# Kernel optimization log

Measured on AMD Instinct MI355X. Metric: run time of the kernel, lower is better.

Reference implementation:

```python
import jax, jax.numpy as jnp
import numpy as np

N = 8192            # number of ROIs
FEAT = 255          # num_classes(151) + embed_dim(100) + pos_dim(4)
HID = 64
PRE_NMS = 6000      # eval-mode pre_nms_topn
POST_NMS = 300      # eval-mode post_nms_topn
NMS_THRESH = 0.7


def setup_inputs() -> dict:
    key = jax.random.key(0)
    ks = jax.random.split(key, 12)
    # rois: [N,5] = (im_ind, x1, y1, x2, y2), valid boxes in a 1024x1024 image
    x1 = jax.random.uniform(ks[0], (N,)) * 900.0
    y1 = jax.random.uniform(ks[1], (N,)) * 900.0
    w = jax.random.uniform(ks[2], (N,)) * 120.0 + 4.0
    h = jax.random.uniform(ks[3], (N,)) * 120.0 + 4.0
    rois = jnp.stack([jnp.zeros((N,)), x1, y1, x1 + w, y1 + h], axis=1).astype(jnp.float32)
    roi_feat = jax.random.normal(ks[4], (N, FEAT), dtype=jnp.float32)
    s = 0.05
    return {
        "rois": rois,
        "roi_feat": roi_feat,
        "W_sub1": jax.random.normal(ks[5], (FEAT, HID), jnp.float32) * s,
        "b_sub1": jnp.zeros((HID,), jnp.float32),
        "W_sub2": jax.random.normal(ks[6], (HID, HID), jnp.float32) * s,
        "b_sub2": jnp.zeros((HID,), jnp.float32),
        "W_obj1": jax.random.normal(ks[7], (FEAT, HID), jnp.float32) * s,
        "b_obj1": jnp.zeros((HID,), jnp.float32),
        "W_obj2": jax.random.normal(ks[8], (HID, HID), jnp.float32) * s,
        "b_obj2": jnp.zeros((HID,), jnp.float32),
    }


def _iou_matrix(boxes):
    # boxes: [K,4] (x1,y1,x2,y2) -> [K,K] IoU
    x1, y1, x2, y2 = boxes[:, 0], boxes[:, 1], boxes[:, 2], boxes[:, 3]
    area = (x2 - x1) * (y2 - y1)
    ix1 = jnp.maximum(x1[:, None], x1[None, :])
    iy1 = jnp.maximum(y1[:, None], y1[None, :])
    ix2 = jnp.minimum(x2[:, None], x2[None, :])
    iy2 = jnp.minimum(y2[:, None], y2[None, :])
    inter = jnp.maximum(ix2 - ix1, 0.0) * jnp.maximum(iy2 - iy1, 0.0)
    return inter / (area[:, None] + area[None, :] - inter + 1e-8)


def reference(rois, roi_feat, W_sub1, b_sub1, W_sub2, b_sub2,
              W_obj1, b_obj1, W_obj2, b_obj2):
    # Original detaches roi_feat before the bilinear head.
    f = jax.lax.stop_gradient(roi_feat)
    x_sub = jnp.maximum(f @ W_sub1 + b_sub1, 0.0) @ W_sub2 + b_sub2  # [N,64]
    x_obj = jnp.maximum(f @ W_obj1 + b_obj1, 0.0) @ W_obj2 + b_obj2  # [N,64]
    scores = jax.nn.sigmoid(x_sub @ x_obj.T)                          # [N,N]

    n = scores.shape[0]
    # exclude self-pairs (sub == obj)
    diag = jnp.arange(n)
    flat = scores.at[diag, diag].set(-1.0).reshape(-1)

    # pre-NMS top-k over all N*N pairs (sorted descending)
    top_s, top_i = jax.lax.top_k(flat, PRE_NMS)
    sub = top_i // n
    obj = top_i % n

    boxes = jax.lax.stop_gradient(rois[:, 1:5])
    bs, bo = boxes[sub], boxes[obj]
    # union box of each (sub,obj) pair for relation NMS
    union = jnp.concatenate([jnp.minimum(bs[:, :2], bo[:, :2]),
                             jnp.maximum(bs[:, 2:], bo[:, 2:])], axis=1)  # [PRE,4]
    iou = _iou_matrix(union)                                              # [PRE,PRE]
    # non-greedy (matrix) NMS: suppress i if any higher-ranked j overlaps > thresh
    higher = jnp.triu(jnp.ones((PRE_NMS, PRE_NMS), bool), k=1)  # [j,i] true when j < i
    suppressed = jnp.any((iou > NMS_THRESH) & higher, axis=0)
    kept_scores = jnp.where(suppressed, -1.0, top_s)

    post_s, post_k = jax.lax.top_k(kept_scores, POST_NMS)
    rel_inds = jnp.stack([sub[post_k], obj[post_k]], axis=1)  # [POST,2]
    return rel_inds, post_s
```

## Files before the change

### kernel.cpp

```cpp
#include <hip/hip_runtime.h>
#include <math.h>

#define NB    8192
#define FEAT  255
#define HID   64
#define TOPK  6000
#define POSTK 300
#define BINS  8192
#define BSHIFT 19
#define CAP   131072
#define CAPLIM 49152
#define SLACK 1
#define TSEL  500
#define SAMPF 16
#define JSLICES 128
#define LCAP  2048
#define NMS_ICH 64

typedef __attribute__((ext_vector_type(8))) short bf16x8;
typedef __attribute__((ext_vector_type(4))) float f32x4;
typedef __attribute__((ext_vector_type(4))) double f64x4;

__device__ __forceinline__ unsigned binOf(float x) {
    unsigned u = __float_as_uint(x);
    u = (u & 0x80000000u) ? ~u : (u | 0x80000000u);
    return u >> BSHIFT;
}

__device__ __forceinline__ unsigned short f2bf(float f) {
    unsigned u = __float_as_uint(f);
    return (unsigned short)((u + 0x7fffu + ((u >> 16) & 1u)) >> 16);
}

__global__ __launch_bounds__(256) void mlp_kernel(
    const float* __restrict__ feat,
    const float* __restrict__ W1s, const float* __restrict__ b1s,
    const float* __restrict__ W2s, const float* __restrict__ b2s,
    const float* __restrict__ W1o, const float* __restrict__ b1o,
    const float* __restrict__ W2o, const float* __restrict__ b2o,
    double* __restrict__ Xs64, double* __restrict__ Xo64,
    unsigned short* __restrict__ Xsb, unsigned short* __restrict__ Xob)
{
    __shared__ float  fl[16 * 258];
    __shared__ double hl[2][16][65];

    int tid  = threadIdx.x;
    int lane = tid & 63;
    int w    = tid >> 6;
    int a16  = lane & 15;
    int kq   = lane >> 4;
    int net  = w & 1;
    int p    = w >> 1;
    int rbase = blockIdx.x * 16;

    const float* fsrc = feat + (size_t)rbase * FEAT;
    for (int idx = tid; idx < 16 * FEAT; idx += 256) {
        int r = idx / FEAT;
        int k = idx - r * FEAT;
        fl[r * 258 + k] = fsrc[idx];
    }
    if (tid < 16) fl[tid * 258 + 255] = 0.0f;
    __syncthreads();

    const float* W1 = net ? W1o : W1s;
    const float* B1 = net ? b1o : b1s;
    const float* W2 = net ? W2o : W2s;
    const float* B2 = net ? b2o : b2s;
    double*       X  = net ? Xo64 : Xs64;
    unsigned short* Xb = net ? Xob : Xsb;

    int c0 = (2 * p) * 16 + a16;
    int c1 = (2 * p + 1) * 16 + a16;

    f64x4 acc0 = {0, 0, 0, 0}, acc1 = {0, 0, 0, 0};
#pragma unroll 4
    for (int ks = 0; ks < 63; ++ks) {
        int k = ks * 4 + kq;
        double av = (double)fl[a16 * 258 + k];
        double b0 = (double)W1[k * HID + c0];
        double b1 = (double)W1[k * HID + c1];
        acc0 = __builtin_amdgcn_mfma_f64_16x16x4f64(av, b0, acc0, 0, 0, 0);
        acc1 = __builtin_amdgcn_mfma_f64_16x16x4f64(av, b1, acc1, 0, 0, 0);
    }
    {
        int k = 252 + kq;
        double av = (double)fl[a16 * 258 + k];
        double b0 = 0.0, b1 = 0.0;
        if (k < FEAT) {
            b0 = (double)W1[k * HID + c0];
            b1 = (double)W1[k * HID + c1];
        }
        acc0 = __builtin_amdgcn_mfma_f64_16x16x4f64(av, b0, acc0, 0, 0, 0);
        acc1 = __builtin_amdgcn_mfma_f64_16x16x4f64(av, b1, acc1, 0, 0, 0);
    }

    {
        double bb0 = (double)B1[c0], bb1 = (double)B1[c1];
#pragma unroll
        for (int i = 0; i < 4; ++i) {
            int r = kq * 4 + i;
            double v0 = acc0[i] + bb0;
            double v1 = acc1[i] + bb1;
            hl[net][r][c0] = v0 > 0.0 ? v0 : 0.0;
            hl[net][r][c1] = v1 > 0.0 ? v1 : 0.0;
        }
    }
    __syncthreads();

    f64x4 x0 = {0, 0, 0, 0}, x1 = {0, 0, 0, 0};
#pragma unroll 4
    for (int ks = 0; ks < 16; ++ks) {
        int k = ks * 4 + kq;
        double av = hl[net][a16][k];
        double b0 = (double)W2[k * HID + c0];
        double b1 = (double)W2[k * HID + c1];
        x0 = __builtin_amdgcn_mfma_f64_16x16x4f64(av, b0, x0, 0, 0, 0);
        x1 = __builtin_amdgcn_mfma_f64_16x16x4f64(av, b1, x1, 0, 0, 0);
    }

    {
        double bb0 = (double)B2[c0], bb1 = (double)B2[c1];
#pragma unroll
        for (int i = 0; i < 4; ++i) {
            int r = kq * 4 + i;
            double v0 = x0[i] + bb0;
            double v1 = x1[i] + bb1;
            size_t o0 = (size_t)(rbase + r) * HID + c0;
            size_t o1 = (size_t)(rbase + r) * HID + c1;
            X[o0] = v0; X[o1] = v1;
            Xb[o0] = f2bf((float)v0);
            Xb[o1] = f2bf((float)v1);
        }
    }
}

__global__ __launch_bounds__(256) void mfma_hist(
    const unsigned short* __restrict__ Xsb, const unsigned short* __restrict__ Xob,
    unsigned* __restrict__ ghist, unsigned* __restrict__ ctrl)
{
    __shared__ unsigned hist[BINS];
    __shared__ unsigned csum[256];
    __shared__ bool win_s;
    int tid = threadIdx.x;
    for (int i = tid; i < BINS; i += 256) hist[i] = 0u;
    __syncthreads();

    int lane = tid & 63;
    int wave = tid >> 6;
    int quad = lane >> 4;
    int l16  = lane & 15;
    int r0 = blockIdx.y * 128 + (wave >> 1) * 64;
    int c0 = blockIdx.x * 128 + (wave & 1) * 64;

    f32x4 acc[4][4];
    bf16x8 afr[2][4], bfr[2][4];
#pragma unroll
    for (int kc = 0; kc < 2; ++kc)
#pragma unroll
        for (int t = 0; t < 4; ++t) {
            afr[kc][t] = *(const bf16x8*)(Xsb + (size_t)(r0 + t * 16 + l16) * HID + kc * 32 + quad * 8);
            bfr[kc][t] = *(const bf16x8*)(Xob + (size_t)(c0 + t * 16 + l16) * HID + kc * 32 + quad * 8);
        }
#pragma unroll
    for (int ti = 0; ti < 4; ++ti)
#pragma unroll
        for (int tj = 0; tj < 4; ++tj) acc[ti][tj] = (f32x4){0, 0, 0, 0};
#pragma unroll
    for (int kc = 0; kc < 2; ++kc)
#pragma unroll
        for (int ti = 0; ti < 4; ++ti)
#pragma unroll
            for (int tj = 0; tj < 4; ++tj)
                acc[ti][tj] = __builtin_amdgcn_mfma_f32_16x16x32_bf16(
                    afr[kc][ti], bfr[kc][tj], acc[ti][tj], 0, 0, 0);

#pragma unroll
    for (int ti = 0; ti < 4; ++ti)
#pragma unroll
        for (int tj = 0; tj < 4; ++tj)
#pragma unroll
            for (int i = 0; i < 4; ++i) {
                int r = r0 + ti * 16 + quad * 4 + i;
                int c = c0 + tj * 16 + l16;
                float v = acc[ti][tj][i];
                if (v > 0.0f && r != c)
                    atomicAdd(&hist[binOf(v)], 1u);
            }

    __syncthreads();
    for (int i = tid; i < BINS; i += 256) {
        unsigned h = hist[i];
        if (h) atomicAdd(&ghist[i], h);
    }

    __syncthreads();
    if (tid == 0) {
        __threadfence();
        unsigned done = atomicAdd(&ctrl[3], 1u);
        win_s = (done == gridDim.x * gridDim.y - 1u);
    }
    __syncthreads();
    if (!win_s) return;

    for (int i = tid; i < BINS; i += 256)
        hist[i] = __hip_atomic_load(&ghist[i], __ATOMIC_RELAXED, __HIP_MEMORY_SCOPE_AGENT);
    __syncthreads();

    int base = tid * (BINS / 256);
    unsigned s = 0;
    for (int i = 0; i < BINS / 256; ++i) s += hist[base + i];
    csum[tid] = s;
    __syncthreads();
    if (tid == 0) {
        unsigned run = 0;
        for (int c = 255; c >= 0; --c) { run += csum[c]; csum[c] = run; }
    }
    __syncthreads();

    unsigned above = (tid == 255) ? 0u : csum[tid + 1];
    unsigned prev = above;
    for (int b = base + BINS / 256 - 1; b >= base; --b) {
        unsigned cur = prev + hist[b];
        if (cur >= TSEL && prev < TSEL) {
            unsigned bstar = (unsigned)b;
            unsigned bt = bstar >= SLACK ? bstar - SLACK : 0;
            unsigned cnt = cur;
            for (unsigned bb = bstar; bb-- > bt;) cnt += hist[bb];
            while ((unsigned)SAMPF * cnt > CAPLIM && bt < bstar) { cnt -= hist[bt]; bt++; }
            ctrl[1] = bt;
            unsigned key = bt << BSHIFT;
            unsigned fbits;
            if (key == 0u) fbits = 0xff800000u;
            else fbits = (key & 0x80000000u) ? (key ^ 0x80000000u) : ~key;
            ctrl[2] = fbits;
            break;
        }
        prev = cur;
    }
}

__global__ __launch_bounds__(256) void mfma_filter(
    const unsigned short* __restrict__ Xsb, const unsigned short* __restrict__ Xob,
    unsigned* __restrict__ ctrl, unsigned* __restrict__ cidx)
{
    __shared__ unsigned lcnt;
    __shared__ unsigned gbase;
    __shared__ unsigned lbuf[LCAP];
    float vt = __uint_as_float(ctrl[2]);
    int tid = threadIdx.x;
    if (tid == 0) lcnt = 0;

    int lane = tid & 63;
    int wave = tid >> 6;
    int quad = lane >> 4;
    int l16  = lane & 15;
    int r0 = blockIdx.y * 128 + (wave >> 1) * 64;
    int cb = blockIdx.x * 256 + (wave & 1) * 64;

    bf16x8 afr[2][4];
#pragma unroll
    for (int kc = 0; kc < 2; ++kc)
#pragma unroll
        for (int t = 0; t < 4; ++t)
            afr[kc][t] = *(const bf16x8*)(Xsb + (size_t)(r0 + t * 16 + l16) * HID + kc * 32 + quad * 8);

    bf16x8 b0[2], b1[2];
    {
        int col0 = cb + l16;
        int col1 = cb + 16 + l16;
#pragma unroll
        for (int kc = 0; kc < 2; ++kc) {
            b0[kc] = *(const bf16x8*)(Xob + (size_t)col0 * HID + kc * 32 + quad * 8);
            b1[kc] = *(const bf16x8*)(Xob + (size_t)col1 * HID + kc * 32 + quad * 8);
        }
    }

    __syncthreads();

#pragma unroll
    for (int q = 0; q < 8; ++q) {
        int ct = q >> 2, tj = q & 3;
        int c0 = cb + ct * 128;
        int cj = c0 + tj * 16 + l16;
        bool nodiag = (r0 != c0);

        bf16x8 b2[2];
        if (q < 6) {
            int q2 = q + 2;
            int col2 = cb + (q2 >> 2) * 128 + (q2 & 3) * 16 + l16;
#pragma unroll
            for (int kc = 0; kc < 2; ++kc)
                b2[kc] = *(const bf16x8*)(Xob + (size_t)col2 * HID + kc * 32 + quad * 8);
        }

        f32x4 acc[4];
#pragma unroll
        for (int ti = 0; ti < 4; ++ti) acc[ti] = (f32x4){0, 0, 0, 0};
#pragma unroll
        for (int kc = 0; kc < 2; ++kc)
#pragma unroll
            for (int ti = 0; ti < 4; ++ti)
                acc[ti] = __builtin_amdgcn_mfma_f32_16x16x32_bf16(
                    afr[kc][ti], b0[kc], acc[ti], 0, 0, 0);

        unsigned hm = 0u;
#pragma unroll
        for (int ti = 0; ti < 4; ++ti)
#pragma unroll
            for (int i = 0; i < 4; ++i) {
                bool hit = acc[ti][i] >= vt;
                if (!nodiag) {
                    int r = r0 + ti * 16 + quad * 4 + i;
                    hit = hit && (r != cj);
                }
                hm |= hit ? (1u << (ti * 4 + i)) : 0u;
            }

        if (__any(hm != 0u)) {
#pragma unroll
            for (int ti = 0; ti < 4; ++ti)
#pragma unroll
                for (int i = 0; i < 4; ++i) {
                    if (hm & (1u << (ti * 4 + i))) {
                        int r = r0 + ti * 16 + quad * 4 + i;
                        unsigned rc = (unsigned)r * (unsigned)NB + (unsigned)cj;
                        unsigned p = atomicAdd(&lcnt, 1u);
                        if (p < LCAP) {
                            lbuf[p] = rc;
                        } else {
                            unsigned g = atomicAdd(&ctrl[0], 1u);
                            if (g < CAP) cidx[g] = rc;
                        }
                    }
                }
        }

        if (q < 6) {
            b0[0] = b1[0]; b0[1] = b1[1];
            b1[0] = b2[0]; b1[1] = b2[1];
        } else if (q == 6) {
            b0[0] = b1[0]; b0[1] = b1[1];
        }
    }

    __syncthreads();
    unsigned n = lcnt; if (n > LCAP) n = LCAP;
    if (tid == 0 && n) gbase = atomicAdd(&ctrl[0], n);
    __syncthreads();
    for (unsigned i = tid; i < n; i += 256u) {
        unsigned p = gbase + i;
        if (p < CAP) cidx[p] = lbuf[i];
    }
}

__global__ __launch_bounds__(256) void refine_kernel(
    const unsigned* __restrict__ ctrl, const unsigned* __restrict__ cidx,
    const double* __restrict__ Xs64, const double* __restrict__ Xo64,
    double* __restrict__ cval)
{
    unsigned M = ctrl[0];
    if (M > CAP) M = CAP;
    unsigned nw = gridDim.x * 4u;
    int lane = threadIdx.x & 63;
    for (unsigned w = blockIdx.x * 4u + (threadIdx.x >> 6); w < M; w += nw) {
        unsigned id = cidx[w];
        unsigned r = id >> 13, c = id & (NB - 1);
        double p = Xs64[(size_t)r * HID + lane] * Xo64[(size_t)c * HID + lane];
#pragma unroll
        for (int s = 32; s > 0; s >>= 1) p += __shfl_xor(p, s);
        if (lane == 0) cval[w] = (r == c) ? -1.0 : p;
    }
}

__global__ __launch_bounds__(256) void rank_count(
    const unsigned* __restrict__ ctrl,
    const double* __restrict__ cval, const unsigned* __restrict__ cidx,
    unsigned* __restrict__ rank)
{
    unsigned M = ctrl[0];
    if (M > CAP) M = CAP;

    unsigned slice = blockIdx.y;
    unsigned jbeg = (unsigned)(((unsigned long long)slice * M) / JSLICES);
    unsigned jend = (unsigned)(((unsigned long long)(slice + 1) * M) / JSLICES);

    __shared__ double  lv[256];
    __shared__ unsigned li[256];

    for (unsigned itile = blockIdx.x; itile * 1024u < M; itile += gridDim.x) {
        unsigned i0 = itile * 1024u + threadIdx.x;
        double v[4];
        unsigned id[4];
        unsigned cnt[4] = {0, 0, 0, 0};
#pragma unroll
        for (int k = 0; k < 4; ++k) {
            unsigned idx = i0 + (unsigned)k * 256u;
            bool a = idx < M;
            v[k]  = a ? cval[idx] : 0.0;
            id[k] = a ? cidx[idx] : 0u;
        }

        for (unsigned base = jbeg; base < jend; base += 256u) {
            unsigned j = base + threadIdx.x;
            if (j < jend) { lv[threadIdx.x] = cval[j]; li[threadIdx.x] = cidx[j]; }
            __syncthreads();
            unsigned lim = jend - base; if (lim > 256u) lim = 256u;
            for (unsigned e = 0; e < lim; ++e) {
                double ev = lv[e];
                unsigned ei = li[e];
#pragma unroll
                for (int k = 0; k < 4; ++k)
                    cnt[k] += (ev > v[k]) || (ev == v[k] && ei < id[k]);
            }
            __syncthreads();
        }
#pragma unroll
        for (int k = 0; k < 4; ++k) {
            unsigned idx = i0 + (unsigned)k * 256u;
            if (idx < M && cnt[k]) atomicAdd(&rank[idx], cnt[k]);
        }
    }
}

__global__ __launch_bounds__(256) void rank_scatter_prep(
    const unsigned* __restrict__ ctrl,
    const double* __restrict__ cval, const unsigned* __restrict__ cidx,
    const unsigned* __restrict__ rank, const float* __restrict__ rois,
    double* __restrict__ sval, unsigned* __restrict__ sidx,
    double* __restrict__ ub)
{
    unsigned M = ctrl[0];
    if (M > CAP) M = CAP;
    unsigned stride = gridDim.x * 256u;
    for (unsigned t = blockIdx.x * 256u + threadIdx.x; t < M; t += stride) {
        unsigned rk = rank[t];
        if (rk < TOPK) {
            unsigned id = cidx[t];
            sval[rk] = cval[t];
            sidx[rk] = id;
            unsigned s = id >> 13, o = id & (NB - 1);
            const float* bs = rois + (size_t)s * 5;
            const float* bo = rois + (size_t)o * 5;
            double x1 = fmin((double)bs[1], (double)bo[1]);
            double y1 = fmin((double)bs[2], (double)bo[2]);
            double x2 = fmax((double)bs[3], (double)bo[3]);
            double y2 = fmax((double)bs[4], (double)bo[4]);
            double area = (x2 - x1) * (y2 - y1);
            double* u = ub + (size_t)rk * 5;
            u[0] = x1; u[1] = y1; u[2] = x2; u[3] = y2; u[4] = 0.7 * area;
        }
    }
}

__global__ __launch_bounds__(256) void nms_kernel(
    const double* __restrict__ ub, unsigned* sup)
{
    int jb = blockIdx.x;
    int ic = blockIdx.y;
    int ibase = ic * NMS_ICH;
    if (ibase >= TOPK) return;
    if (ibase >= jb * 256 + 255) return;

    __shared__ double L[NMS_ICH][5];
    int tid = threadIdx.x;
    int icount = TOPK - ibase; if (icount > NMS_ICH) icount = NMS_ICH;
    for (int q = tid; q < icount * 5; q += 256)
        L[q / 5][q % 5] = ub[(size_t)ibase * 5 + q];
    __syncthreads();

    int j = jb * 256 + tid;
    if (j >= TOPK) return;
    int lim = j - ibase; if (lim > icount) lim = icount;
    if (lim <= 0) return;

    const double* u = ub + (size_t)j * 5;
    double x1 = u[0], y1 = u[1], x2 = u[2], y2 = u[3], pa = u[4];
    bool flag = false;
    for (int e = 0; e < lim; ++e) {
        double ix1 = fmax(L[e][0], x1);
        double iy1 = fmax(L[e][1], y1);
        double ix2 = fmin(L[e][2], x2);
        double iy2 = fmin(L[e][3], y2);
        double iw = ix2 - ix1; iw = iw > 0.0 ? iw : 0.0;
        double ih = iy2 - iy1; ih = ih > 0.0 ? ih : 0.0;
        flag |= (1.7 * (iw * ih) > pa + L[e][4] + 7e-9);
    }
    if (flag) sup[j] = 1u;
}

__global__ __launch_bounds__(1024) void finalize_kernel(
    const unsigned* __restrict__ sup, const double* __restrict__ sval,
    const unsigned* __restrict__ sidx, float* __restrict__ out)
{
    __shared__ unsigned wsum[16];
    __shared__ unsigned red[16];
    __shared__ unsigned bases[2];
    __shared__ unsigned totalu_s;
    int tid  = threadIdx.x;
    int lane = tid & 63;
    int w    = tid >> 6;

    unsigned s = 0;
    for (int i = tid; i < TOPK; i += 1024) s += (sup[i] == 0u);
#pragma unroll
    for (int st = 32; st > 0; st >>= 1) s += __shfl_down(s, st);
    if (lane == 0) red[w] = s;
    __syncthreads();
    if (tid == 0) {
        unsigned tot = 0;
        for (int i = 0; i < 16; ++i) tot += red[i];
        totalu_s = tot; bases[0] = 0; bases[1] = 0;
    }
    __syncthreads();
    unsigned totalu = totalu_s;

    for (int c = 0; c < (TOPK + 1023) / 1024; ++c) {
        int idx = c * 1024 + tid;
        int valid = TOPK - c * 1024; if (valid > 1024) valid = 1024;
        unsigned f = (idx < TOPK && sup[idx] == 0u) ? 1u : 0u;
        unsigned long long m = __ballot(f != 0u);
        if (lane == 0) wsum[w] = (unsigned)__popcll(m);
        __syncthreads();
        unsigned wbase = 0, ctot = 0;
        for (int i = 0; i < 16; ++i) {
            unsigned v = wsum[i];
            if (i < w) wbase += v;
            ctot += v;
        }
        unsigned e = wbase + (unsigned)__popcll(m & ((1ull << lane) - 1ull));
        if (idx < TOPK) {
            unsigned pos = f ? (bases[0] + e)
                             : (totalu + bases[1] + (unsigned)tid - e);
            if (pos < POSTK) {
                unsigned id = sidx[idx];
                unsigned sb = id >> 13, ob = id & (NB - 1);
                out[2 * pos]     = (float)sb;
                out[2 * pos + 1] = (float)ob;
                double sg = f ? 1.0 / (1.0 + exp(-sval[idx])) : -1.0;
                out[2 * POSTK + pos] = (float)sg;
            }
        }
        __syncthreads();
        if (tid == 0) {
            bases[0] += ctot;
            bases[1] += (unsigned)valid - ctot;
        }
        __syncthreads();
    }
}

extern "C" void kernel_launch(void* const* d_in, const int* in_sizes, int n_in,
                              void* d_out, int out_size, void* d_ws, size_t ws_size,
                              hipStream_t stream)
{
    const float* rois = (const float*)d_in[0];
    const float* feat = (const float*)d_in[1];
    const float* W1s  = (const float*)d_in[2];
    const float* b1s  = (const float*)d_in[3];
    const float* W2s  = (const float*)d_in[4];
    const float* b2s  = (const float*)d_in[5];
    const float* W1o  = (const float*)d_in[6];
    const float* b1o  = (const float*)d_in[7];
    const float* W2o  = (const float*)d_in[8];
    const float* b2o  = (const float*)d_in[9];

    char* ws = (char*)d_ws;
    size_t off = 0;
    auto alloc = [&](size_t bytes) -> void* {
        off = (off + 255) & ~(size_t)255;
        void* p = ws + off;
        off += bytes;
        return p;
    };

    unsigned* ghist = (unsigned*)alloc((size_t)BINS * 4);
    unsigned* ctrl  = (unsigned*)alloc(256);
    unsigned* sup   = (unsigned*)alloc((size_t)6144 * 4);
    unsigned* rank  = (unsigned*)alloc((size_t)CAP * 4);
    size_t zero_bytes = off;

    double* Xs64 = (double*)alloc((size_t)NB * HID * 8);
    double* Xo64 = (double*)alloc((size_t)NB * HID * 8);
    unsigned short* Xsb = (unsigned short*)alloc((size_t)NB * HID * 2);
    unsigned short* Xob = (unsigned short*)alloc((size_t)NB * HID * 2);
    double* cval = (double*)alloc((size_t)CAP * 8);
    unsigned* cidx = (unsigned*)alloc((size_t)CAP * 4);
    double* svalv = (double*)alloc((size_t)TOPK * 8);
    unsigned* sidxv = (unsigned*)alloc((size_t)TOPK * 4);
    double* ub   = (double*)alloc((size_t)TOPK * 5 * 8);

    hipMemsetAsync(d_ws, 0, zero_bytes, stream);

    mlp_kernel<<<NB / 16, 256, 0, stream>>>(feat, W1s, b1s, W2s, b2s,
                                            W1o, b1o, W2o, b2o,
                                            Xs64, Xo64, Xsb, Xob);
    mfma_hist<<<dim3(4, 64), 256, 0, stream>>>(Xsb, Xob, ghist, ctrl);
    mfma_filter<<<dim3(32, 64), 256, 0, stream>>>(Xsb, Xob, ctrl, cidx);
    refine_kernel<<<2048, 256, 0, stream>>>(ctrl, cidx, Xs64, Xo64, cval);
    rank_count<<<dim3(16, JSLICES), 256, 0, stream>>>(ctrl, cval, cidx, rank);
    rank_scatter_prep<<<512, 256, 0, stream>>>(ctrl, cval, cidx, rank, rois,
                                               svalv, sidxv, ub);
    nms_kernel<<<dim3((TOPK + 255) / 256, (TOPK + NMS_ICH - 1) / NMS_ICH), 256, 0, stream>>>(ub, sup);
    finalize_kernel<<<1, 1024, 0, stream>>>(sup, svalv, sidxv, (float*)d_out);
}
```

Before: 225.3 us.

## Fuse refine, scatter and finalize stages into neighbouring kernels via last-block pattern

Candidate double-precision rescoring moves into the filter kernel, so each block refines the candidates it just appended; rank zeroing is also done there and drops out of the memset. The rank scatter and union-box prep now run in the last-finishing block of rank_count, found through an atomic counter. Finalize likewise runs in the last-finishing block of the NMS kernel. This removes three kernel launches and their inter-kernel gaps. In exchange, the scatter and finalize work is serialized onto one 256-thread block, and correctness depends on threadfence and atomic visibility.

```diff
diff --git a/kernel.cpp b/kernel.cpp
--- a/kernel.cpp
+++ b/kernel.cpp
@@ -241,7 +241,9 @@
 
 __global__ __launch_bounds__(256) void mfma_filter(
     const unsigned short* __restrict__ Xsb, const unsigned short* __restrict__ Xob,
-    unsigned* __restrict__ ctrl, unsigned* __restrict__ cidx)
+    unsigned* __restrict__ ctrl, unsigned* __restrict__ cidx,
+    const double* __restrict__ Xs64, const double* __restrict__ Xo64,
+    double* __restrict__ cval, unsigned* __restrict__ rank)
 {
     __shared__ unsigned lcnt;
     __shared__ unsigned gbase;
@@ -329,7 +331,15 @@
                             lbuf[p] = rc;
                         } else {
                             unsigned g = atomicAdd(&ctrl[0], 1u);
-                            if (g < CAP) cidx[g] = rc;
+                            if (g < CAP) {
+                                cidx[g] = rc;
+                                const double* xr = Xs64 + (size_t)r * HID;
+                                const double* xc = Xo64 + (size_t)cj * HID;
+                                double a64 = 0.0;
+                                for (int k = 0; k < HID; ++k) a64 += xr[k] * xc[k];
+                                cval[g] = a64;
+                                rank[g] = 0u;
+                            }
                         }
                     }
                 }
@@ -351,34 +361,29 @@
         unsigned p = gbase + i;
         if (p < CAP) cidx[p] = lbuf[i];
     }
-}
-
-__global__ __launch_bounds__(256) void refine_kernel(
-    const unsigned* __restrict__ ctrl, const unsigned* __restrict__ cidx,
-    const double* __restrict__ Xs64, const double* __restrict__ Xo64,
-    double* __restrict__ cval)
+
+    for (unsigned i = (unsigned)wave; i < n; i += 4u) {
+        unsigned g = gbase + i;
+        if (g < CAP) {
+            unsigned rc = lbuf[i];
+            unsigned r = rc >> 13, c = rc & (NB - 1u);
+            double pr = Xs64[(size_t)r * HID + lane] * Xo64[(size_t)c * HID + lane];
+#pragma unroll
+            for (int s = 32; s > 0; s >>= 1) pr += __shfl_xor(pr, s);
+            if (lane == 0) { cval[g] = pr; rank[g] = 0u; }
+        }
+    }
+}
+
+__global__ __launch_bounds__(256) void rank_count(
+    unsigned* __restrict__ ctrl,
+    const double* __restrict__ cval, const unsigned* __restrict__ cidx,
+    unsigned* __restrict__ rank, const float* __restrict__ rois,
+    double* __restrict__ sval, unsigned* __restrict__ sidx,
+    double* __restrict__ ub)
 {
     unsigned M = ctrl[0];
     if (M > CAP) M = CAP;
-    unsigned nw = gridDim.x * 4u;
-    int lane = threadIdx.x & 63;
-    for (unsigned w = blockIdx.x * 4u + (threadIdx.x >> 6); w < M; w += nw) {
-        unsigned id = cidx[w];
-        unsigned r = id >> 13, c = id & (NB - 1);
-        double p = Xs64[(size_t)r * HID + lane] * Xo64[(size_t)c * HID + lane];
-#pragma unroll
-        for (int s = 32; s > 0; s >>= 1) p += __shfl_xor(p, s);
-        if (lane == 0) cval[w] = (r == c) ? -1.0 : p;
-    }
-}
-
-__global__ __launch_bounds__(256) void rank_count(
-    const unsigned* __restrict__ ctrl,
-    const double* __restrict__ cval, const unsigned* __restrict__ cidx,
-    unsigned* __restrict__ rank)
-{
-    unsigned M = ctrl[0];
-    if (M > CAP) M = CAP;
 
     unsigned slice = blockIdx.y;
     unsigned jbeg = (unsigned)(((unsigned long long)slice * M) / JSLICES);
@@ -386,6 +391,7 @@
 
     __shared__ double  lv[256];
     __shared__ unsigned li[256];
+    __shared__ bool win_s;
 
     for (unsigned itile = blockIdx.x; itile * 1024u < M; itile += gridDim.x) {
         unsigned i0 = itile * 1024u + threadIdx.x;
@@ -420,20 +426,18 @@
             if (idx < M && cnt[k]) atomicAdd(&rank[idx], cnt[k]);
         }
     }
-}
-
-__global__ __launch_bounds__(256) void rank_scatter_prep(
-    const unsigned* __restrict__ ctrl,
-    const double* __restrict__ cval, const unsigned* __restrict__ cidx,
-    const unsigned* __restrict__ rank, const float* __restrict__ rois,
-    double* __restrict__ sval, unsigned* __restrict__ sidx,
-    double* __restrict__ ub)
-{
-    unsigned M = ctrl[0];
-    if (M > CAP) M = CAP;
-    unsigned stride = gridDim.x * 256u;
-    for (unsigned t = blockIdx.x * 256u + threadIdx.x; t < M; t += stride) {
-        unsigned rk = rank[t];
+
+    __syncthreads();
+    if (threadIdx.x == 0) {
+        __threadfence();
+        unsigned done = atomicAdd(&ctrl[4], 1u);
+        win_s = (done == gridDim.x * gridDim.y - 1u);
+    }
+    __syncthreads();
+    if (!win_s) return;
+
+    for (unsigned t = threadIdx.x; t < M; t += 256u) {
+        unsigned rk = __hip_atomic_load(&rank[t], __ATOMIC_RELAXED, __HIP_MEMORY_SCOPE_AGENT);
         if (rk < TOPK) {
             unsigned id = cidx[t];
             sval[rk] = cval[t];
@@ -453,76 +457,88 @@
 }
 
 __global__ __launch_bounds__(256) void nms_kernel(
-    const double* __restrict__ ub, unsigned* sup)
+    const double* __restrict__ ub, unsigned* sup, unsigned* __restrict__ ctrl,
+    const double* __restrict__ sval, const unsigned* __restrict__ sidx,
+    float* __restrict__ out)
 {
+    __shared__ double L[NMS_ICH][5];
+    __shared__ bool win_s;
     int jb = blockIdx.x;
     int ic = blockIdx.y;
     int ibase = ic * NMS_ICH;
-    if (ibase >= TOPK) return;
-    if (ibase >= jb * 256 + 255) return;
-
-    __shared__ double L[NMS_ICH][5];
     int tid = threadIdx.x;
-    int icount = TOPK - ibase; if (icount > NMS_ICH) icount = NMS_ICH;
-    for (int q = tid; q < icount * 5; q += 256)
-        L[q / 5][q % 5] = ub[(size_t)ibase * 5 + q];
-    __syncthreads();
-
-    int j = jb * 256 + tid;
-    if (j >= TOPK) return;
-    int lim = j - ibase; if (lim > icount) lim = icount;
-    if (lim <= 0) return;
-
-    const double* u = ub + (size_t)j * 5;
-    double x1 = u[0], y1 = u[1], x2 = u[2], y2 = u[3], pa = u[4];
-    bool flag = false;
-    for (int e = 0; e < lim; ++e) {
-        double ix1 = fmax(L[e][0], x1);
-        double iy1 = fmax(L[e][1], y1);
-        double ix2 = fmin(L[e][2], x2);
-        double iy2 = fmin(L[e][3], y2);
-        double iw = ix2 - ix1; iw = iw > 0.0 ? iw : 0.0;
-        double ih = iy2 - iy1; ih = ih > 0.0 ? ih : 0.0;
-        flag |= (1.7 * (iw * ih) > pa + L[e][4] + 7e-9);
-    }
-    if (flag) sup[j] = 1u;
-}
-
-__global__ __launch_bounds__(1024) void finalize_kernel(
-    const unsigned* __restrict__ sup, const double* __restrict__ sval,
-    const unsigned* __restrict__ sidx, float* __restrict__ out)
-{
-    __shared__ unsigned wsum[16];
-    __shared__ unsigned red[16];
+
+    bool blk_active = (ibase < TOPK) && (ibase < jb * 256 + 255);
+    if (blk_active) {
+        int icount = TOPK - ibase; if (icount > NMS_ICH) icount = NMS_ICH;
+        for (int q = tid; q < icount * 5; q += 256)
+            L[q / 5][q % 5] = ub[(size_t)ibase * 5 + q];
+        __syncthreads();
+
+        int j = jb * 256 + tid;
+        if (j < TOPK) {
+            int lim = j - ibase; if (lim > icount) lim = icount;
+            if (lim > 0) {
+                const double* u = ub + (size_t)j * 5;
+                double x1 = u[0], y1 = u[1], x2 = u[2], y2 = u[3], pa = u[4];
+                bool flag = false;
+                for (int e = 0; e < lim; ++e) {
+                    double ix1 = fmax(L[e][0], x1);
+                    double iy1 = fmax(L[e][1], y1);
+                    double ix2 = fmin(L[e][2], x2);
+                    double iy2 = fmin(L[e][3], y2);
+                    double iw = ix2 - ix1; iw = iw > 0.0 ? iw : 0.0;
+                    double ih = iy2 - iy1; ih = ih > 0.0 ? ih : 0.0;
+                    flag |= (1.7 * (iw * ih) > pa + L[e][4] + 7e-9);
+                }
+                if (flag)
+                    __hip_atomic_store(&sup[j], 1u, __ATOMIC_RELAXED, __HIP_MEMORY_SCOPE_AGENT);
+            }
+        }
+    }
+
+    __syncthreads();
+    if (tid == 0) {
+        __threadfence();
+        unsigned done = atomicAdd(&ctrl[5], 1u);
+        win_s = (done == gridDim.x * gridDim.y - 1u);
+    }
+    __syncthreads();
+    if (!win_s) return;
+
+    __shared__ unsigned wsum[4];
+    __shared__ unsigned red[4];
     __shared__ unsigned bases[2];
     __shared__ unsigned totalu_s;
-    int tid  = threadIdx.x;
     int lane = tid & 63;
     int w    = tid >> 6;
 
     unsigned s = 0;
-    for (int i = tid; i < TOPK; i += 1024) s += (sup[i] == 0u);
+    for (int i = tid; i < TOPK; i += 256)
+        s += (__hip_atomic_load(&sup[i], __ATOMIC_RELAXED, __HIP_MEMORY_SCOPE_AGENT) == 0u);
 #pragma unroll
     for (int st = 32; st > 0; st >>= 1) s += __shfl_down(s, st);
     if (lane == 0) red[w] = s;
     __syncthreads();
     if (tid == 0) {
-        unsigned tot = 0;
-        for (int i = 0; i < 16; ++i) tot += red[i];
+        unsigned tot = red[0] + red[1] + red[2] + red[3];
         totalu_s = tot; bases[0] = 0; bases[1] = 0;
     }
     __syncthreads();
     unsigned totalu = totalu_s;
 
-    for (int c = 0; c < (TOPK + 1023) / 1024; ++c) {
-        int idx = c * 1024 + tid;
-        int valid = TOPK - c * 1024; if (valid > 1024) valid = 1024;
-        unsigned f = (idx < TOPK && sup[idx] == 0u) ? 1u : 0u;
+    for (int c = 0; c < (TOPK + 255) / 256; ++c) {
+        int idx = c * 256 + tid;
+        int valid = TOPK - c * 256; if (valid > 256) valid = 256;
+        unsigned f = (idx < TOPK &&
+                      __hip_atomic_load(&sup[idx], __ATOMIC_RELAXED, __HIP_MEMORY_SCOPE_AGENT) == 0u)
+                     ? 1u : 0u;
         unsigned long long m = __ballot(f != 0u);
         if (lane == 0) wsum[w] = (unsigned)__popcll(m);
         __syncthreads();
         unsigned wbase = 0, ctot = 0;
-        for (int i = 0; i < 16; ++i) {
+#pragma unroll
+        for (int i = 0; i < 4; ++i) {
             unsigned v = wsum[i];
             if (i < w) wbase += v;
             ctot += v;
@@ -576,9 +592,9 @@
     unsigned* ghist = (unsigned*)alloc((size_t)BINS * 4);
     unsigned* ctrl  = (unsigned*)alloc(256);
     unsigned* sup   = (unsigned*)alloc((size_t)6144 * 4);
+    size_t zero_bytes = off;
+
     unsigned* rank  = (unsigned*)alloc((size_t)CAP * 4);
-    size_t zero_bytes = off;
-
     double* Xs64 = (double*)alloc((size_t)NB * HID * 8);
     double* Xo64 = (double*)alloc((size_t)NB * HID * 8);
     unsigned short* Xsb = (unsigned short*)alloc((size_t)NB * HID * 2);
@@ -589,17 +605,16 @@
     unsigned* sidxv = (unsigned*)alloc((size_t)TOPK * 4);
     double* ub   = (double*)alloc((size_t)TOPK * 5 * 8);
 
-    hipMemsetAsync(d_ws, 0, zero_bytes, stream);
+    (void)hipMemsetAsync(d_ws, 0, zero_bytes, stream);
 
     mlp_kernel<<<NB / 16, 256, 0, stream>>>(feat, W1s, b1s, W2s, b2s,
                                             W1o, b1o, W2o, b2o,
                                             Xs64, Xo64, Xsb, Xob);
     mfma_hist<<<dim3(4, 64), 256, 0, stream>>>(Xsb, Xob, ghist, ctrl);
-    mfma_filter<<<dim3(32, 64), 256, 0, stream>>>(Xsb, Xob, ctrl, cidx);
-    refine_kernel<<<2048, 256, 0, stream>>>(ctrl, cidx, Xs64, Xo64, cval);
-    rank_count<<<dim3(16, JSLICES), 256, 0, stream>>>(ctrl, cval, cidx, rank);
-    rank_scatter_prep<<<512, 256, 0, stream>>>(ctrl, cval, cidx, rank, rois,
-                                               svalv, sidxv, ub);
-    nms_kernel<<<dim3((TOPK + 255) / 256, (TOPK + NMS_ICH - 1) / NMS_ICH), 256, 0, stream>>>(ub, sup);
-    finalize_kernel<<<1, 1024, 0, stream>>>(sup, svalv, sidxv, (float*)d_out);
-}
+    mfma_filter<<<dim3(32, 64), 256, 0, stream>>>(Xsb, Xob, ctrl, cidx,
+                                                  Xs64, Xo64, cval, rank);
+    rank_count<<<dim3(16, JSLICES), 256, 0, stream>>>(ctrl, cval, cidx, rank,
+                                                      rois, svalv, sidxv, ub);
+    nms_kernel<<<dim3((TOPK + 255) / 256, (TOPK + NMS_ICH - 1) / NMS_ICH), 256, 0, stream>>>(
+        ub, sup, ctrl, svalv, sidxv, (float*)d_out);
+}
```

Measured after the change: 327.6 us. +45.4%, slower.
